# Kernel optimization log

Measured on AMD Instinct MI355X. Metric: run time of the kernel, lower is better.

## Reference

```python
import jax, jax.numpy as jnp
import numpy as np

ELEM_ID = 3.0  # mocked pw element id for 'agentLemming'
B, C, H, W = 16, 20, 512, 512


def _step(world, fall_left):
    # torch.roll semantics: get_above = roll(+1, H-axis), get_below = roll(-1, H-axis),
    # get_left = roll(+1, W-axis), get_right = roll(-1, W-axis)
    shift_w = 1 if fall_left else -1
    density = world[:, 1:2]                                   # [B,1,H,W]
    is_element = world[:, 0:1] == ELEM_ID                     # pw.get_bool(world,'agentLemming')
    density_forward = jnp.roll(density, shift_w, axis=3)
    density_above = jnp.roll(density, 1, axis=2)
    density_forward_above = jnp.roll(density_above, shift_w, axis=3)
    does_become_above = (is_element
                         & (density_forward - density >= 0)
                         & (density_above - density < 0)
                         & (density_forward_above - density < 0))
    does_become_below = jnp.roll(does_become_above, -1, axis=2)
    world_above = jnp.roll(world, 1, axis=2)
    world_below = jnp.roll(world, -1, axis=2)
    a = does_become_above.astype(world.dtype)                 # broadcasts [B,1,H,W] over C
    b = does_become_below.astype(world.dtype)
    # interp2: (~a & ~b)*if_false + a*if_a + b*if_b  (sums if both switches fire, as in torch)
    return (1.0 - a) * (1.0 - b) * world + a * world_above + b * world_below


def setup_inputs() -> dict:
    key = jax.random.key(0)
    k1, k2, k3, k4, k5 = jax.random.split(key, 5)
    world = jax.random.normal(k1, (B, C, H, W), dtype=jnp.float32)
    # channel 0 holds integer element ids; id 3 == agentLemming
    elem_ids = jax.random.randint(k5, (B, 1, H, W), 0, 10).astype(jnp.float32)
    world = world.at[:, 0:1].set(elem_ids)
    rand_movement = jax.random.uniform(k2, (B, 1, H, W), dtype=jnp.float32)
    rand_interact = jax.random.uniform(k3, (B, 1, H, W), dtype=jnp.float32)
    rand_element = jax.random.uniform(k4, (B, 1, H, W), dtype=jnp.float32)
    return {"world": world, "rand_movement": rand_movement,
            "rand_interact": rand_interact, "rand_element": rand_element}


def reference(world, rand_movement, rand_interact, rand_element):
    # rand_* are unpacked from info but unused by BehaviorLemming
    world = _step(world, fall_left=True)
    world = _step(world, fall_left=False)
    return world
```

## Files before the change

### kernel.cpp

```cpp
#include <hip/hip_runtime.h>

#define Bn 16
#define Cn 20
#define Hn 512
#define Wn 512
#define HWn (Hn*Wn)
#define Rn 16
#define CGn 4
#define CPG 5

typedef float f32x4 __attribute__((ext_vector_type(4)));

__device__ unsigned char g_a1[(size_t)Bn*HWn];
__device__ unsigned char g_a2[(size_t)Bn*HWn];

__global__ __launch_bounds__(256) void mask1_kernel(const float* __restrict__ world) {
    int idx = blockIdx.x * 256 + threadIdx.x;
    int w = idx & (Wn - 1);
    int h = (idx >> 9) & (Hn - 1);
    int b = idx >> 18;
    const float* e = world + (size_t)b * Cn * HWn;
    const float* d = e + HWn;
    int wm = (w - 1) & (Wn - 1);
    int hm = (h - 1) & (Hn - 1);
    float dc  = d[h  * Wn + w];
    float df  = d[h  * Wn + wm];
    float da  = d[hm * Wn + w];
    float dfa = d[hm * Wn + wm];
    bool a = (e[h * Wn + w] == 3.0f) & (df - dc >= 0.0f) & (da - dc < 0.0f) & (dfa - dc < 0.0f);
    g_a1[idx] = (unsigned char)a;
}

__device__ __forceinline__ float stepval(const float* __restrict__ p,
                                         const unsigned char* __restrict__ a1p,
                                         int r, int wc) {
    int rm = (r - 1) & (Hn - 1), rp = (r + 1) & (Hn - 1);
    unsigned char a  = a1p[r  * Wn + wc];
    unsigned char bb = a1p[rp * Wn + wc];
    float v;
    if (a)       { v = p[rm * Wn + wc]; if (bb) v += p[rp * Wn + wc]; }
    else if (bb) { v = p[rp * Wn + wc]; }
    else         { v = p[r  * Wn + wc]; }
    return v;
}

__global__ __launch_bounds__(256) void mask2_kernel(const float* __restrict__ world) {
    int idx = blockIdx.x * 256 + threadIdx.x;
    int w = idx & (Wn - 1);
    int h = (idx >> 9) & (Hn - 1);
    int b = idx >> 18;
    const float* e = world + (size_t)b * Cn * HWn;
    const float* d = e + HWn;
    const unsigned char* a1p = g_a1 + (size_t)b * HWn;
    int wp = (w + 1) & (Wn - 1);
    int hm = (h - 1) & (Hn - 1);
    float I0   = stepval(e, a1p, h,  w);
    float I1c  = stepval(d, a1p, h,  w);
    float I1f  = stepval(d, a1p, h,  wp);
    float I1a  = stepval(d, a1p, hm, w);
    float I1fa = stepval(d, a1p, hm, wp);
    bool a = (I0 == 3.0f) & (I1f - I1c >= 0.0f) & (I1a - I1c < 0.0f) & (I1fa - I1c < 0.0f);
    g_a2[idx] = (unsigned char)a;
}

__global__ __launch_bounds__(256) void final_kernel(const float* __restrict__ world,
                                                    float* __restrict__ out) {
    int t    = blockIdx.x * 256 + threadIdx.x;
    int wq   = t & 127;
    int cg   = (t >> 7) & 3;
    int tile = (t >> 9) & 31;
    int b    = t >> 14;
    int w    = wq * 4;
    int h0   = tile * Rn;

    const unsigned char* a1p = g_a1 + (size_t)b * HWn;
    const unsigned char* a2p = g_a2 + (size_t)b * HWn;

    unsigned int a1r[Rn + 3];
    unsigned int a2r[Rn + 1];
#pragma unroll
    for (int r = 0; r < Rn + 3; r++) {
        int h = (h0 - 1 + r) & (Hn - 1);
        a1r[r] = *(const unsigned int*)(a1p + (size_t)h * Wn + w);
    }
#pragma unroll
    for (int r = 0; r < Rn + 1; r++) {
        int h = (h0 + r) & (Hn - 1);
        a2r[r] = *(const unsigned int*)(a2p + (size_t)h * Wn + w);
    }

    const unsigned int ONE = 0x01010101u;
    unsigned int cw[Rn];
#pragma unroll
    for (int r = 0; r < Rn; r++) {
        unsigned int rm1 = a1r[r], r0 = a1r[r + 1], rp1 = a1r[r + 2], rp2 = a1r[r + 3];
        unsigned int s0 = a2r[r], s1 = a2r[r + 1];
        unsigned int z   = (s0 | s1) ^ ONE;
        unsigned int cm2 = s0 & rm1;
        unsigned int cm1 = (s0 & (rm1 ^ ONE) & (r0 ^ ONE)) | (z & r0);
        unsigned int c0  = (s0 & r0) + (z & (r0 ^ ONE) & (rp1 ^ ONE)) + (s1 & rp1);
        unsigned int cp1 = (z & rp1) | (s1 & (rp1 ^ ONE) & (rp2 ^ ONE));
        unsigned int cp2 = s1 & rp2;
        cw[r] = cm2 | (cm1 << 1) | ((c0 & ONE) << 2) | (((c0 >> 1) & ONE) << 3)
                    | (cp1 << 4) | (cp2 << 5);
    }

    const float* base  = world + ((size_t)b * Cn + (size_t)cg * CPG) * HWn + w;
    float*       obase = out   + ((size_t)b * Cn + (size_t)cg * CPG) * HWn + w;

#pragma unroll 1
    for (int c = 0; c < CPG; c++) {
        const float* p = base  + (size_t)c * HWn;
        float*       q = obase + (size_t)c * HWn;
        f32x4 xm2 = *(const f32x4*)(p + (size_t)((h0 - 2) & (Hn - 1)) * Wn);
        f32x4 xm1 = *(const f32x4*)(p + (size_t)((h0 - 1) & (Hn - 1)) * Wn);
        f32x4 x0  = *(const f32x4*)(p + (size_t)h0 * Wn);
        f32x4 xp1 = *(const f32x4*)(p + (size_t)(h0 + 1) * Wn);
#pragma unroll
        for (int r = 0; r < Rn; r++) {
            f32x4 xp2 = *(const f32x4*)(p + (size_t)((h0 + r + 2) & (Hn - 1)) * Wn);
            unsigned int cwr = cw[r];
            f32x4 o;
#pragma unroll
            for (int j = 0; j < 4; j++) {
                unsigned int u = (cwr >> (8 * j)) & 0xffu;
                float fm2 = (float)(u & 1u);
                float fm1 = (float)((u >> 1) & 1u);
                float f0  = (float)((u >> 2) & 3u);
                float fp1 = (float)((u >> 4) & 1u);
                float fp2 = (float)((u >> 5) & 1u);
                o[j] = fm2 * xm2[j] + fm1 * xm1[j] + f0 * x0[j] + fp1 * xp1[j] + fp2 * xp2[j];
            }
            __builtin_nontemporal_store(o, (f32x4*)(q + (size_t)(h0 + r) * Wn));
            xm2 = xm1; xm1 = x0; x0 = xp1; xp1 = xp2;
        }
    }
}

extern "C" void kernel_launch(void* const* d_in, const int* in_sizes, int n_in,
                              void* d_out, int out_size, void* d_ws, size_t ws_size,
                              hipStream_t stream) {
    const float* world = (const float*)d_in[0];
    float* out = (float*)d_out;

    mask1_kernel<<<(Bn * HWn) / 256, 256, 0, stream>>>(world);
    mask2_kernel<<<(Bn * HWn) / 256, 256, 0, stream>>>(world);
    final_kernel<<<(Bn * (Hn / Rn) * CGn * (Wn / 4)) / 256, 256, 0, stream>>>(world, out);
}
```

Baseline: 647.8 us.

## Halve final-kernel row tile, stream mask rows, and swizzle blocks across XCDs

```diff
diff --git a/kernel.cpp b/kernel.cpp
--- a/kernel.cpp
+++ b/kernel.cpp
@@ -5,9 +5,10 @@
 #define Hn 512
 #define Wn 512
 #define HWn (Hn*Wn)
-#define Rn 16
+#define Rn 8
 #define CGn 4
 #define CPG 5
+#define NBLK ((Bn * (Hn / Rn) * CGn * (Wn / 4)) / 256)
 
 typedef float f32x4 __attribute__((ext_vector_type(4)));
 
@@ -63,46 +64,44 @@
     g_a2[idx] = (unsigned char)a;
 }
 
-__global__ __launch_bounds__(256) void final_kernel(const float* __restrict__ world,
-                                                    float* __restrict__ out) {
-    int t    = blockIdx.x * 256 + threadIdx.x;
+__global__ __launch_bounds__(256, 4) void final_kernel(const float* __restrict__ world,
+                                                       float* __restrict__ out) {
+    int bid = blockIdx.x;
+    int lb  = (bid & 7) * (NBLK / 8) + (bid >> 3);
+    int t   = lb * 256 + threadIdx.x;
     int wq   = t & 127;
     int cg   = (t >> 7) & 3;
-    int tile = (t >> 9) & 31;
-    int b    = t >> 14;
+    int tile = (t >> 9) & (Hn / Rn - 1);
+    int b    = t >> (9 + 6);
     int w    = wq * 4;
     int h0   = tile * Rn;
 
     const unsigned char* a1p = g_a1 + (size_t)b * HWn;
     const unsigned char* a2p = g_a2 + (size_t)b * HWn;
 
-    unsigned int a1r[Rn + 3];
-    unsigned int a2r[Rn + 1];
-#pragma unroll
-    for (int r = 0; r < Rn + 3; r++) {
-        int h = (h0 - 1 + r) & (Hn - 1);
-        a1r[r] = *(const unsigned int*)(a1p + (size_t)h * Wn + w);
-    }
-#pragma unroll
-    for (int r = 0; r < Rn + 1; r++) {
-        int h = (h0 + r) & (Hn - 1);
-        a2r[r] = *(const unsigned int*)(a2p + (size_t)h * Wn + w);
-    }
-
     const unsigned int ONE = 0x01010101u;
     unsigned int cw[Rn];
+    {
+        unsigned int a1w0 = *(const unsigned int*)(a1p + (size_t)((h0 - 1) & (Hn - 1)) * Wn + w);
+        unsigned int a1w1 = *(const unsigned int*)(a1p + (size_t)h0 * Wn + w);
+        unsigned int a1w2 = *(const unsigned int*)(a1p + (size_t)((h0 + 1) & (Hn - 1)) * Wn + w);
+        unsigned int a2w0 = *(const unsigned int*)(a2p + (size_t)h0 * Wn + w);
 #pragma unroll
-    for (int r = 0; r < Rn; r++) {
-        unsigned int rm1 = a1r[r], r0 = a1r[r + 1], rp1 = a1r[r + 2], rp2 = a1r[r + 3];
-        unsigned int s0 = a2r[r], s1 = a2r[r + 1];
-        unsigned int z   = (s0 | s1) ^ ONE;
-        unsigned int cm2 = s0 & rm1;
-        unsigned int cm1 = (s0 & (rm1 ^ ONE) & (r0 ^ ONE)) | (z & r0);
-        unsigned int c0  = (s0 & r0) + (z & (r0 ^ ONE) & (rp1 ^ ONE)) + (s1 & rp1);
-        unsigned int cp1 = (z & rp1) | (s1 & (rp1 ^ ONE) & (rp2 ^ ONE));
-        unsigned int cp2 = s1 & rp2;
-        cw[r] = cm2 | (cm1 << 1) | ((c0 & ONE) << 2) | (((c0 >> 1) & ONE) << 3)
-                    | (cp1 << 4) | (cp2 << 5);
+        for (int r = 0; r < Rn; r++) {
+            unsigned int a1w3 = *(const unsigned int*)(a1p + (size_t)((h0 + r + 2) & (Hn - 1)) * Wn + w);
+            unsigned int a2w1 = *(const unsigned int*)(a2p + (size_t)((h0 + r + 1) & (Hn - 1)) * Wn + w);
+            unsigned int rm1 = a1w0, r0 = a1w1, rp1 = a1w2, rp2 = a1w3;
+            unsigned int s0 = a2w0, s1 = a2w1;
+            unsigned int z   = (s0 | s1) ^ ONE;
+            unsigned int cm2 = s0 & rm1;
+            unsigned int cm1 = (s0 & (rm1 ^ ONE) & (r0 ^ ONE)) | (z & r0);
+            unsigned int c0  = (s0 & r0) + (z & (r0 ^ ONE) & (rp1 ^ ONE)) + (s1 & rp1);
+            unsigned int cp1 = (z & rp1) | (s1 & (rp1 ^ ONE) & (rp2 ^ ONE));
+            unsigned int cp2 = s1 & rp2;
+            cw[r] = cm2 | (cm1 << 1) | ((c0 & ONE) << 2) | (((c0 >> 1) & ONE) << 3)
+                        | (cp1 << 4) | (cp2 << 5);
+            a1w0 = a1w1; a1w1 = a1w2; a1w2 = a1w3; a2w0 = a2w1;
+        }
     }
 
     const float* base  = world + ((size_t)b * Cn + (size_t)cg * CPG) * HWn + w;
@@ -145,5 +144,5 @@
 
     mask1_kernel<<<(Bn * HWn) / 256, 256, 0, stream>>>(world);
     mask2_kernel<<<(Bn * HWn) / 256, 256, 0, stream>>>(world);
-    final_kernel<<<(Bn * (Hn / Rn) * CGn * (Wn / 4)) / 256, 256, 0, stream>>>(world, out);
+    final_kernel<<<NBLK, 256, 0, stream>>>(world, out);
 }
```

New measurement: 730.6 us. +12.8%, slower.
